# Performance work log

Hardware: AMD Instinct MI355X
Metric: run time of the kernel (lower is better)

## Reference

```python
import jax, jax.numpy as jnp
from jax import lax
import numpy as np

KSIZE = 7
LOSS_WEIGHT = 1.0


def _box_sum(x, k):
    # sliding-window sum over last two dims, window k x k, stride 1, VALID
    return lax.reduce_window(x, 0.0, lax.add, (1, 1, k, k), (1, 1, 1, 1), 'VALID')


def setup_inputs() -> dict:
    key = jax.random.key(0)
    k1, k2 = jax.random.split(key)
    shape = (32, 3, 512, 512)
    return {
        'net_output': jax.random.normal(k1, shape, dtype=jnp.float32),
        'gt': jax.random.normal(k2, shape, dtype=jnp.float32),
    }


def reference(net_output, gt):
    k = KSIZE
    n = float(k * k)
    pad = (k - 1) // 2

    # residual_sr: sum of abs channel differences -> [B,1,H,W]
    residual = jnp.sum(jnp.abs(gt - net_output), axis=1, keepdims=True)

    # patch-level weight: unbiased variance over (C,H,W), keepdim, ** (1/5)
    patch_w = jnp.var(residual, axis=(1, 2, 3), keepdims=True, ddof=1) ** 0.2

    # pixel-level weight: unbiased local variance in k x k window (reflect pad)
    # computed via box sums: var = (S2 - S1^2/n) / (n-1)  -- O(1) memory traffic
    rp = jnp.pad(residual, ((0, 0), (0, 0), (pad, pad), (pad, pad)), mode='reflect')
    s1 = _box_sum(rp, k)
    s2 = _box_sum(rp * rp, k)
    pixel_w = (s2 - s1 * s1 / n) / (n - 1.0)

    overall_weight = patch_w * pixel_w  # [B,1,H,W], broadcasts over C

    out = overall_weight * net_output
    g = overall_weight * gt
    # L1 criterion (init default), mean reduction
    return jnp.mean(jnp.abs(out - g)) * LOSS_WEIGHT
```

## Files before the change

### kernel.cpp

```cpp
#include <hip/hip_runtime.h>

#define BB 32
#define CC 3
#define HH 512
#define WW 512
#define KS 7
#define PADR 3
#define HW (HH*WW)
#define TS 32
#define TP (TS + KS - 1)
#define TBX (WW / TS)
#define NTILE (TBX * TBX)
#define NBLK (NTILE * BB)

__global__ __launch_bounds__(256) void fused_kernel(const float* __restrict__ net,
                                                    const float* __restrict__ gt,
                                                    float4* __restrict__ partials) {
    __shared__ float tile[TP][TP + 2];
    __shared__ float h1[TP][TS], h2[TP][TS];

    int b  = blockIdx.z;
    int r0 = blockIdx.y * TS, c0 = blockIdx.x * TS;
    const float* nb = net + (size_t)b * CC * HW;
    const float* gb = gt  + (size_t)b * CC * HW;
    int tid = threadIdx.y * 32 + threadIdx.x;

    for (int i = tid; i < TP * TP; i += 256) {
        int rr = i / TP, cc = i - rr * TP;
        int gr = r0 + rr - PADR; gr = (gr < 0) ? -gr : ((gr >= HH) ? 2*HH - 2 - gr : gr);
        int gc = c0 + cc - PADR; gc = (gc < 0) ? -gc : ((gc >= WW) ? 2*WW - 2 - gc : gc);
        int off = gr * WW + gc;
        float r = fabsf(gb[off]        - nb[off])
                + fabsf(gb[HW + off]   - nb[HW + off])
                + fabsf(gb[2*HW + off] - nb[2*HW + off]);
        tile[rr][cc] = r;
    }
    __syncthreads();

    for (int i = tid; i < TP * TS; i += 256) {
        int rr = i / TS, cc = i - rr * TS;
        float a = 0.f, aa = 0.f;
        #pragma unroll
        for (int k = 0; k < KS; k++) { float v = tile[rr][cc + k]; a += v; aa += v * v; }
        h1[rr][cc] = a; h2[rr][cc] = aa;
    }
    __syncthreads();

    float sr = 0.f, sr2 = 0.f, tot = 0.f;
    for (int rr = threadIdx.y; rr < TS; rr += 8) {
        int cc = threadIdx.x;
        float s1 = 0.f, s2 = 0.f;
        #pragma unroll
        for (int k = 0; k < KS; k++) { s1 += h1[rr + k][cc]; s2 += h2[rr + k][cc]; }
        float pw = (s2 - s1 * s1 * (1.0f / 49.0f)) * (1.0f / 48.0f);
        float r  = tile[rr + PADR][cc + PADR];
        sr += r; sr2 += r * r; tot += pw * r;
    }

    #pragma unroll
    for (int off = 32; off > 0; off >>= 1) {
        sr  += __shfl_down(sr,  off);
        sr2 += __shfl_down(sr2, off);
        tot += __shfl_down(tot, off);
    }
    __shared__ float p0[4], p1[4], p2[4];
    int lane = tid & 63, wid = tid >> 6;
    if (lane == 0) { p0[wid] = sr; p1[wid] = sr2; p2[wid] = tot; }
    __syncthreads();
    if (tid == 0) {
        int blkid = (b * TBX + blockIdx.y) * TBX + blockIdx.x;
        partials[blkid] = make_float4(p0[0] + p0[1] + p0[2] + p0[3],
                                      p1[0] + p1[1] + p1[2] + p1[3],
                                      p2[0] + p2[1] + p2[2] + p2[3], 0.f);
    }
}

__global__ __launch_bounds__(256) void reduce_kernel(const float4* __restrict__ partials,
                                                     double* __restrict__ pb) {
    int b = blockIdx.x;
    float4 v = partials[b * NTILE + threadIdx.x];
    double s1 = v.x, s2 = v.y, t = v.z;
    #pragma unroll
    for (int off = 32; off > 0; off >>= 1) {
        s1 += __shfl_down(s1, off);
        s2 += __shfl_down(s2, off);
        t  += __shfl_down(t,  off);
    }
    __shared__ double q0[4], q1[4], q2[4];
    int lane = threadIdx.x & 63, wid = threadIdx.x >> 6;
    if (lane == 0) { q0[wid] = s1; q1[wid] = s2; q2[wid] = t; }
    __syncthreads();
    if (threadIdx.x == 0) {
        double S1 = q0[0] + q0[1] + q0[2] + q0[3];
        double S2 = q1[0] + q1[1] + q1[2] + q1[3];
        double T  = q2[0] + q2[1] + q2[2] + q2[3];
        double N  = (double)HW;
        double var = (S2 - S1 * S1 / N) / (N - 1.0);
        pb[b] = pow(var, 0.2) * T;
    }
}

__global__ void final_kernel(const double* __restrict__ pb, float* __restrict__ out) {
    double v = (threadIdx.x < BB) ? pb[threadIdx.x] : 0.0;
    #pragma unroll
    for (int off = 32; off > 0; off >>= 1) v += __shfl_down(v, off);
    if (threadIdx.x == 0) out[0] = (float)(v / ((double)BB * CC * HW));
}

extern "C" void kernel_launch(void* const* d_in, const int* in_sizes, int n_in,
                              void* d_out, int out_size, void* d_ws, size_t ws_size,
                              hipStream_t stream) {
    const float* net = (const float*)d_in[0];
    const float* gt  = (const float*)d_in[1];
    float* out = (float*)d_out;

    char* ws = (char*)d_ws;
    float4* partials = (float4*)ws;
    double* pb       = (double*)(ws + NBLK * sizeof(float4));

    dim3 grid(TBX, TBX, BB);
    dim3 blk(32, 8);
    fused_kernel<<<grid, blk, 0, stream>>>(net, gt, partials);
    reduce_kernel<<<BB, NTILE, 0, stream>>>(partials, pb);
    final_kernel<<<1, 64, 0, stream>>>(pb, out);
}
```

Before: 240.9 us.

## Stream row bands with register sliding window and merge reduction kernels

Replaces the 32x32 2D tile (with its 38x38 halo re-read of all six input planes) by 32-row by 256-column strips. Each thread owns one column and streams rows through a double-buffered shared row buffer, keeping the vertical 7-row window of horizontal sums in registers. This cuts halo re-reads from about 41% to about 22% and software-prefetches the next row's loads. The two small reduction kernels are merged into one 1024-thread finalize kernel, saving a launch. The cost is a __syncthreads per row and fewer, larger blocks (1024 total).

```diff
diff --git a/kernel.cpp b/kernel.cpp
--- a/kernel.cpp
+++ b/kernel.cpp
@@ -4,57 +4,108 @@
 #define CC 3
 #define HH 512
 #define WW 512
-#define KS 7
-#define PADR 3
 #define HW (HH*WW)
-#define TS 32
-#define TP (TS + KS - 1)
-#define TBX (WW / TS)
-#define NTILE (TBX * TBX)
-#define NBLK (NTILE * BB)
+#define BAND 32
+#define SW 256
+#define NBAND (HH/BAND)
+#define NSTRIP (WW/SW)
+#define NBLK (BB*NBAND*NSTRIP)
+
+__device__ __forceinline__ int refl(int x, int n) {
+    x = (x < 0) ? -x : x;
+    return (x >= n) ? (2*n - 2 - x) : x;
+}
 
 __global__ __launch_bounds__(256) void fused_kernel(const float* __restrict__ net,
                                                     const float* __restrict__ gt,
                                                     float4* __restrict__ partials) {
-    __shared__ float tile[TP][TP + 2];
-    __shared__ float h1[TP][TS], h2[TP][TS];
+    const int b = blockIdx.z, band = blockIdx.y, strip = blockIdx.x;
+    const int bs = band * BAND, be = bs + BAND;
+    const int c0 = strip * SW;
+    const int tid = threadIdx.x;
 
-    int b  = blockIdx.z;
-    int r0 = blockIdx.y * TS, c0 = blockIdx.x * TS;
+    __shared__ float resbuf[2][SW + 8];
+
     const float* nb = net + (size_t)b * CC * HW;
     const float* gb = gt  + (size_t)b * CC * HW;
-    int tid = threadIdx.y * 32 + threadIdx.x;
 
-    for (int i = tid; i < TP * TP; i += 256) {
-        int rr = i / TP, cc = i - rr * TP;
-        int gr = r0 + rr - PADR; gr = (gr < 0) ? -gr : ((gr >= HH) ? 2*HH - 2 - gr : gr);
-        int gc = c0 + cc - PADR; gc = (gc < 0) ? -gc : ((gc >= WW) ? 2*WW - 2 - gc : gc);
-        int off = gr * WW + gc;
-        float r = fabsf(gb[off]        - nb[off])
-                + fabsf(gb[HW + off]   - nb[HW + off])
-                + fabsf(gb[2*HW + off] - nb[2*HW + off]);
-        tile[rr][cc] = r;
+    const int gc0 = refl(c0 - 3 + tid, WW);
+    const bool halo = tid < 6;
+    const int gc1 = halo ? refl(c0 - 3 + SW + tid, WW) : 0;
+
+    float hr1[8], hr2[8], rr[8];
+    float sr = 0.f, sr2 = 0.f, tot = 0.f;
+
+    int ro = refl(bs - 3, HH) * WW;
+    float a0 = nb[ro+gc0], a1 = nb[HW+ro+gc0], a2 = nb[2*HW+ro+gc0];
+    float g0 = gb[ro+gc0], g1 = gb[HW+ro+gc0], g2 = gb[2*HW+ro+gc0];
+    float A0=0, A1=0, A2=0, G0=0, G1=0, G2=0;
+    if (halo) { A0 = nb[ro+gc1]; A1 = nb[HW+ro+gc1]; A2 = nb[2*HW+ro+gc1];
+                G0 = gb[ro+gc1]; G1 = gb[HW+ro+gc1]; G2 = gb[2*HW+ro+gc1]; }
+
+    #pragma unroll
+    for (int p = 0; p < 6; ++p) {
+        const int prow = bs - 3 + p;
+        const int slot = (5 + p) & 7;
+        const int buf  = (p + 1) & 1;
+        float r0v = fabsf(g0-a0) + fabsf(g1-a1) + fabsf(g2-a2);
+        float r1v = 0.f;
+        if (halo) r1v = fabsf(G0-A0) + fabsf(G1-A1) + fabsf(G2-A2);
+        ro = refl(prow + 1, HH) * WW;
+        a0 = nb[ro+gc0]; a1 = nb[HW+ro+gc0]; a2 = nb[2*HW+ro+gc0];
+        g0 = gb[ro+gc0]; g1 = gb[HW+ro+gc0]; g2 = gb[2*HW+ro+gc0];
+        if (halo) { A0 = nb[ro+gc1]; A1 = nb[HW+ro+gc1]; A2 = nb[2*HW+ro+gc1];
+                    G0 = gb[ro+gc1]; G1 = gb[HW+ro+gc1]; G2 = gb[2*HW+ro+gc1]; }
+        resbuf[buf][tid] = r0v;
+        if (halo) resbuf[buf][SW + tid] = r1v;
+        __syncthreads();
+        float s1 = 0.f, s2 = 0.f, own = 0.f;
+        #pragma unroll
+        for (int k = 0; k < 7; ++k) {
+            float v = resbuf[buf][tid + k];
+            s1 += v; s2 += v * v;
+            if (k == 3) own = v;
+        }
+        hr1[slot] = s1; hr2[slot] = s2; rr[slot] = own;
+        if (p >= 3) { sr += own; sr2 += own * own; }
     }
-    __syncthreads();
 
-    for (int i = tid; i < TP * TS; i += 256) {
-        int rr = i / TS, cc = i - rr * TS;
-        float a = 0.f, aa = 0.f;
+    for (int r0 = bs; r0 < be; r0 += 8) {
         #pragma unroll
-        for (int k = 0; k < KS; k++) { float v = tile[rr][cc + k]; a += v; aa += v * v; }
-        h1[rr][cc] = a; h2[rr][cc] = aa;
-    }
-    __syncthreads();
-
-    float sr = 0.f, sr2 = 0.f, tot = 0.f;
-    for (int rr = threadIdx.y; rr < TS; rr += 8) {
-        int cc = threadIdx.x;
-        float s1 = 0.f, s2 = 0.f;
-        #pragma unroll
-        for (int k = 0; k < KS; k++) { s1 += h1[rr + k][cc]; s2 += h2[rr + k][cc]; }
-        float pw = (s2 - s1 * s1 * (1.0f / 49.0f)) * (1.0f / 48.0f);
-        float r  = tile[rr + PADR][cc + PADR];
-        sr += r; sr2 += r * r; tot += pw * r;
+        for (int j = 0; j < 8; ++j) {
+            const int r = r0 + j;
+            const int prow = r + 3;
+            const int slot = (j + 3) & 7;
+            const int buf  = (j + 1) & 1;
+            float r0v = fabsf(g0-a0) + fabsf(g1-a1) + fabsf(g2-a2);
+            float r1v = 0.f;
+            if (halo) r1v = fabsf(G0-A0) + fabsf(G1-A1) + fabsf(G2-A2);
+            ro = refl(prow + 1, HH) * WW;
+            a0 = nb[ro+gc0]; a1 = nb[HW+ro+gc0]; a2 = nb[2*HW+ro+gc0];
+            g0 = gb[ro+gc0]; g1 = gb[HW+ro+gc0]; g2 = gb[2*HW+ro+gc0];
+            if (halo) { A0 = nb[ro+gc1]; A1 = nb[HW+ro+gc1]; A2 = nb[2*HW+ro+gc1];
+                        G0 = gb[ro+gc1]; G1 = gb[HW+ro+gc1]; G2 = gb[2*HW+ro+gc1]; }
+            resbuf[buf][tid] = r0v;
+            if (halo) resbuf[buf][SW + tid] = r1v;
+            __syncthreads();
+            float s1 = 0.f, s2 = 0.f, own = 0.f;
+            #pragma unroll
+            for (int k = 0; k < 7; ++k) {
+                float v = resbuf[buf][tid + k];
+                s1 += v; s2 += v * v;
+                if (k == 3) own = v;
+            }
+            hr1[slot] = s1; hr2[slot] = s2; rr[slot] = own;
+            if (prow < be) { sr += own; sr2 += own * own; }
+            float v1 = 0.f, v2 = 0.f;
+            #pragma unroll
+            for (int k = 0; k < 7; ++k) {
+                v1 += hr1[(j + 5 + k) & 7];
+                v2 += hr2[(j + 5 + k) & 7];
+            }
+            float pw = (v2 - v1 * v1 * (1.0f/49.0f)) * (1.0f/48.0f);
+            tot += pw * rr[j & 7];
+        }
     }
 
     #pragma unroll
@@ -63,48 +114,40 @@
         sr2 += __shfl_down(sr2, off);
         tot += __shfl_down(tot, off);
     }
-    __shared__ float p0[4], p1[4], p2[4];
-    int lane = tid & 63, wid = tid >> 6;
-    if (lane == 0) { p0[wid] = sr; p1[wid] = sr2; p2[wid] = tot; }
+    __shared__ float red[3][4];
+    const int lane = tid & 63, wid = tid >> 6;
+    if (lane == 0) { red[0][wid] = sr; red[1][wid] = sr2; red[2][wid] = tot; }
     __syncthreads();
     if (tid == 0) {
-        int blkid = (b * TBX + blockIdx.y) * TBX + blockIdx.x;
-        partials[blkid] = make_float4(p0[0] + p0[1] + p0[2] + p0[3],
-                                      p1[0] + p1[1] + p1[2] + p1[3],
-                                      p2[0] + p2[1] + p2[2] + p2[3], 0.f);
+        const int blkid = (b * NBAND + band) * NSTRIP + strip;
+        partials[blkid] = make_float4(red[0][0]+red[0][1]+red[0][2]+red[0][3],
+                                      red[1][0]+red[1][1]+red[1][2]+red[1][3],
+                                      red[2][0]+red[2][1]+red[2][2]+red[2][3], 0.f);
     }
 }
 
-__global__ __launch_bounds__(256) void reduce_kernel(const float4* __restrict__ partials,
-                                                     double* __restrict__ pb) {
-    int b = blockIdx.x;
-    float4 v = partials[b * NTILE + threadIdx.x];
-    double s1 = v.x, s2 = v.y, t = v.z;
+__global__ __launch_bounds__(1024) void finalize_kernel(const float4* __restrict__ partials,
+                                                        float* __restrict__ out) {
+    const int t = threadIdx.x;
+    float4 v = partials[t];
+    double s1 = v.x, s2 = v.y, tt = v.z;
     #pragma unroll
-    for (int off = 32; off > 0; off >>= 1) {
-        s1 += __shfl_down(s1, off);
-        s2 += __shfl_down(s2, off);
-        t  += __shfl_down(t,  off);
+    for (int off = 16; off > 0; off >>= 1) {
+        s1 += __shfl_down(s1, off, 32);
+        s2 += __shfl_down(s2, off, 32);
+        tt += __shfl_down(tt, off, 32);
     }
-    __shared__ double q0[4], q1[4], q2[4];
-    int lane = threadIdx.x & 63, wid = threadIdx.x >> 6;
-    if (lane == 0) { q0[wid] = s1; q1[wid] = s2; q2[wid] = t; }
+    __shared__ double L[3][32];
+    if ((t & 31) == 0) { int bb = t >> 5; L[0][bb] = s1; L[1][bb] = s2; L[2][bb] = tt; }
     __syncthreads();
-    if (threadIdx.x == 0) {
-        double S1 = q0[0] + q0[1] + q0[2] + q0[3];
-        double S2 = q1[0] + q1[1] + q1[2] + q1[3];
-        double T  = q2[0] + q2[1] + q2[2] + q2[3];
-        double N  = (double)HW;
-        double var = (S2 - S1 * S1 / N) / (N - 1.0);
-        pb[b] = pow(var, 0.2) * T;
+    if (t < 32) {
+        double S1 = L[0][t], S2 = L[1][t], T = L[2][t];
+        double N = (double)HW;
+        double val = pow((S2 - S1 * S1 / N) / (N - 1.0), 0.2) * T;
+        #pragma unroll
+        for (int off = 16; off > 0; off >>= 1) val += __shfl_down(val, off, 32);
+        if (t == 0) out[0] = (float)(val / ((double)BB * CC * HW));
     }
-}
-
-__global__ void final_kernel(const double* __restrict__ pb, float* __restrict__ out) {
-    double v = (threadIdx.x < BB) ? pb[threadIdx.x] : 0.0;
-    #pragma unroll
-    for (int off = 32; off > 0; off >>= 1) v += __shfl_down(v, off);
-    if (threadIdx.x == 0) out[0] = (float)(v / ((double)BB * CC * HW));
 }
 
 extern "C" void kernel_launch(void* const* d_in, const int* in_sizes, int n_in,
@@ -114,13 +157,9 @@
     const float* gt  = (const float*)d_in[1];
     float* out = (float*)d_out;
 
-    char* ws = (char*)d_ws;
-    float4* partials = (float4*)ws;
-    double* pb       = (double*)(ws + NBLK * sizeof(float4));
+    float4* partials = (float4*)d_ws;
 
-    dim3 grid(TBX, TBX, BB);
-    dim3 blk(32, 8);
-    fused_kernel<<<grid, blk, 0, stream>>>(net, gt, partials);
-    reduce_kernel<<<BB, NTILE, 0, stream>>>(partials, pb);
-    final_kernel<<<1, 64, 0, stream>>>(pb, out);
+    dim3 grid(NSTRIP, NBAND, BB);
+    fused_kernel<<<grid, 256, 0, stream>>>(net, gt, partials);
+    finalize_kernel<<<1, 1024, 0, stream>>>(partials, out);
 }
```

After: 224.1 us. -7.0%, faster.
